# Kernel tuning notes

Hardware: AMD Instinct MI355X
Metric: run time of the kernel (lower is better)

Reference implementation:

```python
import jax, jax.numpy as jnp
import numpy as np

N_HEAD, D_K, D_V, D_MODEL = 8, 64, 64, 512
LN_EPS = 1e-5

def setup_inputs() -> dict:
    key = jax.random.key(0)
    k1, k2, k3 = jax.random.split(key, 3)
    B, C, H, W = 8, D_MODEL, 32, 32
    q = jax.random.normal(k1, (B, C, H, W), dtype=jnp.float32)
    w_qkvs = jax.random.normal(k2, (N_HEAD * D_K, D_MODEL), dtype=jnp.float32) * np.sqrt(2.0 / (D_MODEL + D_K))
    fc_w = jax.random.normal(k3, (D_MODEL, N_HEAD * D_V), dtype=jnp.float32) * np.sqrt(2.0 / (N_HEAD * D_V + D_MODEL))
    fc_b = jnp.zeros((D_MODEL,), dtype=jnp.float32)
    ln_gamma = jnp.ones((D_MODEL,), dtype=jnp.float32)
    ln_beta = jnp.zeros((D_MODEL,), dtype=jnp.float32)
    return {"q": q, "w_qkvs": w_qkvs, "fc_w": fc_w, "fc_b": fc_b,
            "ln_gamma": ln_gamma, "ln_beta": ln_beta}

def reference(q, w_qkvs, fc_w, fc_b, ln_gamma, ln_beta):
    B, C, H, W = q.shape
    L = H * W
    temp = np.sqrt(D_K).astype(np.float32)
    # [B, C, H, W] -> [B, L, C] tokens
    x = q.reshape(B, C, L).transpose(0, 2, 1)
    residual = x
    # shared QKV projection -> per-head [B, h, L, d]
    qh = (x @ w_qkvs.T).reshape(B, L, N_HEAD, D_K).transpose(0, 2, 1, 3)
    # self-attention: q = k = v = qh
    scores = jnp.einsum('bhqd,bhkd->bhqk', qh, qh) / temp
    attn = jax.nn.softmax(scores, axis=-1)  # dropout is identity in eval
    out = jnp.einsum('bhqk,bhkd->bhqd', attn, qh)  # [B, h, L, d_v]
    # merge heads: [B, L, h*d_v]
    out = out.transpose(0, 2, 1, 3).reshape(B, L, N_HEAD * D_V)
    out = out @ fc_w.T + fc_b
    y = out + residual
    mu = jnp.mean(y, axis=-1, keepdims=True)
    var = jnp.mean(jnp.square(y - mu), axis=-1, keepdims=True)
    y = (y - mu) / jnp.sqrt(var + LN_EPS) * ln_gamma + ln_beta
    # raw reshape, matching torch .view(B, -1, H, W)
    return y.reshape(B, -1, H, W)
```

## Files before the change

### kernel.cpp

```cpp
#include <hip/hip_runtime.h>
#include <stdint.h>

#define BATCH 8
#define LTOK 1024
#define DMODEL 512
#define NHEAD 8
#define DHEAD 64

typedef unsigned short u16;
typedef u16 u16x8 __attribute__((ext_vector_type(8)));
typedef short bf16x8 __attribute__((ext_vector_type(8)));
typedef float f32x4 __attribute__((ext_vector_type(4)));

#define MFMA16(a,b,c) __builtin_amdgcn_mfma_f32_16x16x32_bf16((a),(b),(c),0,0,0)

__device__ __forceinline__ float bf2f(u16 x){
  union{unsigned u; float f;} v; v.u = ((unsigned)x)<<16; return v.f;
}
__device__ __forceinline__ u16 f2bf(float f){
  union{float f; unsigned u;} v; v.f = f;
  unsigned r = v.u + 0x7fffu + ((v.u>>16)&1u);
  return (u16)(r>>16);
}

__device__ __forceinline__ void gload_lds16(const u16* g, u16* l){
  __builtin_amdgcn_global_load_lds(
      (const __attribute__((address_space(1))) void*)g,
      (__attribute__((address_space(3))) void*)l,
      16, 0, 0);
}

__global__ __launch_bounds__(256) void convert_k(const float* __restrict__ src,
                                                 u16* __restrict__ dst, int n){
  const int i = (blockIdx.x*256 + threadIdx.x)*8;
  if (i >= n) return;
  u16x8 v;
  #pragma unroll
  for (int j=0;j<8;j++) v[j] = f2bf(src[i+j]);
  *(u16x8*)(dst + i) = v;
}

__global__ __launch_bounds__(256) void transpose_f2b(const float* __restrict__ src,
                                                     u16* __restrict__ dst,
                                                     int R, int C){
  __shared__ __align__(16) u16 t[64][72];
  const int b  = blockIdx.z;
  const int r0 = blockIdx.x*64, c0 = blockIdx.y*64;
  const float* s = src + (size_t)b*R*C;
  u16* d         = dst + (size_t)b*R*C;
  const int tid = threadIdx.x;
  const int row = tid>>3, ch = (tid&7)*8;
  #pragma unroll
  for (int rr=0; rr<64; rr+=32){
    const float* p = s + (size_t)(r0+row+rr)*C + c0 + ch;
    u16x8 v;
    #pragma unroll
    for (int j=0;j<8;j++) v[j] = f2bf(p[j]);
    *(u16x8*)&t[row+rr][ch] = v;
  }
  __syncthreads();
  #pragma unroll
  for (int rr=0; rr<64; rr+=32){
    const int dr = row+rr;
    u16x8 v;
    #pragma unroll
    for (int j=0;j<8;j++) v[j] = t[ch+j][dr];
    *(u16x8*)(d + (size_t)(c0+dr)*R + r0 + ch) = v;
  }
}

__device__ __forceinline__ void stage_gemm(const u16* __restrict__ src,
                                           int row0, int k0, u16* lds, int tid){
  #pragma unroll
  for (int s2=0; s2<2; ++s2){
    const int slot = tid + s2*256;
    const int row = slot>>3, ch8 = slot&7;
    const int k = k0 + ((ch8 ^ (row&7))<<3);
    gload_lds16(src + (size_t)(row0+row)*DMODEL + k, lds + slot*8);
  }
}

__global__ __launch_bounds__(256) void qkv_gemm(const u16* __restrict__ A,
                                                const u16* __restrict__ W,
                                                u16* __restrict__ Kf,
                                                u16* __restrict__ Vf){
  __shared__ __align__(128) u16 sA[2][4096];
  __shared__ __align__(128) u16 sB[2][4096];
  const int m0 = blockIdx.x*64, n0 = blockIdx.y*64;
  const int tid = threadIdx.x, w = tid>>6, lane = tid&63;
  const int wr = w>>1, wc = w&1;
  const int lr = lane&15, lg = lane>>4;
  f32x4 acc[2][2] = {};
  stage_gemm(A, m0, 0, sA[0], tid);
  stage_gemm(W, n0, 0, sB[0], tid);
  int buf = 0;
  for (int kt=0; kt<8; ++kt){
    __syncthreads();
    if (kt < 7){
      stage_gemm(A, m0, (kt+1)*64, sA[buf^1], tid);
      stage_gemm(W, n0, (kt+1)*64, sB[buf^1], tid);
    }
    #pragma unroll
    for (int ks=0; ks<2; ++ks){
      bf16x8 af[2], bfr[2];
      #pragma unroll
      for (int mi=0; mi<2; ++mi){
        const int r = wr*32 + mi*16 + lr;
        af[mi] = *(const bf16x8*)(&sA[buf][(r*64 + ks*32 + lg*8) ^ ((r&7)<<3)]);
      }
      #pragma unroll
      for (int nj=0; nj<2; ++nj){
        const int r = wc*32 + nj*16 + lr;
        bfr[nj] = *(const bf16x8*)(&sB[buf][(r*64 + ks*32 + lg*8) ^ ((r&7)<<3)]);
      }
      #pragma unroll
      for (int mi=0; mi<2; ++mi)
        #pragma unroll
        for (int nj=0; nj<2; ++nj)
          acc[mi][nj] = MFMA16(af[mi], bfr[nj], acc[mi][nj]);
    }
    buf ^= 1;
  }
  #pragma unroll
  for (int mi=0; mi<2; ++mi)
    #pragma unroll
    for (int nj=0; nj<2; ++nj)
      #pragma unroll
      for (int r=0; r<4; ++r){
        const int m = m0 + wr*32 + mi*16 + lg*4 + r;
        const int n = n0 + wc*32 + nj*16 + lr;
        const int bb = m>>10, l = m&1023, hh = n>>6, d = n&63;
        const int bh = bb*NHEAD + hh;
        const int t = l>>6;
        const u16 val = f2bf(acc[mi][nj][r]);
        {
          const int rr = l&63;
          const int fnj = rr>>4, flr = rr&15;
          const int fks = d>>5, flg = (d>>3)&3, fj = d&7;
          Kf[(size_t)(bh*16 + t)*4096 + (fks*4+fnj)*512 + (flg*16+flr)*8 + fj] = val;
        }
        {
          const int ll = l&63;
          const int fks = ll>>5, flg = (ll>>3)&3, fj = ll&7;
          const int fdj = d>>4, flr = d&15;
          Vf[(size_t)(bh*16 + t)*4096 + (fks*4+fdj)*512 + (flg*16+flr)*8 + fj] = val;
        }
      }
}

__global__ __launch_bounds__(256,1) void attn_k(const u16* __restrict__ kf,
                                                const u16* __restrict__ vf,
                                                u16* __restrict__ ao){
  __shared__ __align__(128) u16 sP[16384];
  const int bid = blockIdx.x;
  const int qt = bid >> 6, bh = bid & 63;
  const int b = bh >> 3, h = bh & 7;
  const u16* Kf = kf + (size_t)bh*16*4096;
  const u16* Vf = vf + (size_t)bh*16*4096;
  const int tid = threadIdx.x, w = tid>>6, lane = tid&63;
  const int lr = lane&15, lg = lane>>4;
  const int qtw = qt*4 + w;

  bf16x8 aq[4][2];
  #pragma unroll
  for (int g=0; g<4; ++g)
    #pragma unroll
    for (int ks=0; ks<2; ++ks){
      u16x8 v = *(const u16x8*)(Kf + (size_t)qtw*4096 + (ks*4+g)*512 + lane*8);
      bf16x8 t;
      #pragma unroll
      for (int j=0;j<8;j++) t[j] = (short)f2bf(bf2f(v[j])*0.18033688f);
      aq[g][ks] = t;
    }

  f32x4 o[4][4] = {};
  float lsum[4][4] = {};

  for (int kt=0; kt<16; ++kt){
    const u16* Kt = Kf + (size_t)kt*4096;
    const u16* Vt = Vf + (size_t)kt*4096;
    bf16x8 bk[2][4];
    #pragma unroll
    for (int ks=0; ks<2; ++ks)
      #pragma unroll
      for (int nj=0; nj<4; ++nj)
        bk[ks][nj] = *(const bf16x8*)(Kt + (ks*4+nj)*512 + lane*8);
    #pragma unroll
    for (int g=0; g<4; ++g){
      f32x4 sc[4] = {};
      __builtin_amdgcn_s_setprio(1);
      #pragma unroll
      for (int ks=0; ks<2; ++ks)
        #pragma unroll
        for (int nj=0; nj<4; ++nj)
          sc[nj] = MFMA16(aq[g][ks], bk[ks][nj], sc[nj]);
      __builtin_amdgcn_s_setprio(0);
      const int wp = (w*4+g)*1024;
      #pragma unroll
      for (int nj=0; nj<4; ++nj){
        #pragma unroll
        for (int r=0; r<4; ++r){
          const float p = __builtin_amdgcn_exp2f(sc[nj][r]);
          const unsigned pu = __float_as_uint(p) & 0xFFFF0000u;
          lsum[g][r] += __uint_as_float(pu);
          const int prow = lg*4 + r;
          sP[wp + ((prow*64 + nj*16 + lr) ^ ((prow&7)<<3))] = (u16)(pu>>16);
        }
      }
    }
    asm volatile("s_waitcnt lgkmcnt(0)" ::: "memory");
    bf16x8 bv[2][4];
    #pragma unroll
    for (int ks=0; ks<2; ++ks)
      #pragma unroll
      for (int dj=0; dj<4; ++dj)
        bv[ks][dj] = *(const bf16x8*)(Vt + (ks*4+dj)*512 + lane*8);
    __builtin_amdgcn_s_setprio(1);
    #pragma unroll
    for (int g=0; g<4; ++g){
      const int wp = (w*4+g)*1024;
      #pragma unroll
      for (int ks=0; ks<2; ++ks){
        bf16x8 pa = *(const bf16x8*)(&sP[wp + ((lr*64 + ks*32 + lg*8) ^ ((lr&7)<<3))]);
        #pragma unroll
        for (int dj=0; dj<4; ++dj)
          o[g][dj] = MFMA16(pa, bv[ks][dj], o[g][dj]);
      }
    }
    __builtin_amdgcn_s_setprio(0);
  }

  #pragma unroll
  for (int g=0; g<4; ++g){
    float inv[4];
    #pragma unroll
    for (int r=0; r<4; ++r){
      float s = lsum[g][r];
      s += __shfl_xor(s,1); s += __shfl_xor(s,2);
      s += __shfl_xor(s,4); s += __shfl_xor(s,8);
      inv[r] = __builtin_amdgcn_rcpf(s);
    }
    const int i0 = qtw*64 + g*16;
    #pragma unroll
    for (int dj=0; dj<4; ++dj)
      #pragma unroll
      for (int r=0; r<4; ++r){
        const int l = i0 + lg*4 + r;
        const int d = dj*16 + lr;
        ao[((size_t)(b*LTOK + l))*DMODEL + h*DHEAD + d] = f2bf(o[g][dj][r]*inv[r]);
      }
  }
}

__global__ __launch_bounds__(256) void fc_gemm(const u16* __restrict__ A,
                                               const u16* __restrict__ W,
                                               const float* __restrict__ bias,
                                               const u16* __restrict__ resid,
                                               u16* __restrict__ Y){
  __shared__ __align__(128) u16 sA[2][4096];
  __shared__ __align__(128) u16 sB[2][4096];
  const int m0 = blockIdx.x*64, n0 = blockIdx.y*64;
  const int tid = threadIdx.x, w = tid>>6, lane = tid&63;
  const int wr = w>>1, wc = w&1;
  const int lr = lane&15, lg = lane>>4;
  f32x4 acc[2][2] = {};
  stage_gemm(A, m0, 0, sA[0], tid);
  stage_gemm(W, n0, 0, sB[0], tid);
  int buf = 0;
  for (int kt=0; kt<8; ++kt){
    __syncthreads();
    if (kt < 7){
      stage_gemm(A, m0, (kt+1)*64, sA[buf^1], tid);
      stage_gemm(W, n0, (kt+1)*64, sB[buf^1], tid);
    }
    #pragma unroll
    for (int ks=0; ks<2; ++ks){
      bf16x8 af[2], bfr[2];
      #pragma unroll
      for (int mi=0; mi<2; ++mi){
        const int r = wr*32 + mi*16 + lr;
        af[mi] = *(const bf16x8*)(&sA[buf][(r*64 + ks*32 + lg*8) ^ ((r&7)<<3)]);
      }
      #pragma unroll
      for (int nj=0; nj<2; ++nj){
        const int r = wc*32 + nj*16 + lr;
        bfr[nj] = *(const bf16x8*)(&sB[buf][(r*64 + ks*32 + lg*8) ^ ((r&7)<<3)]);
      }
      #pragma unroll
      for (int mi=0; mi<2; ++mi)
        #pragma unroll
        for (int nj=0; nj<2; ++nj)
          acc[mi][nj] = MFMA16(af[mi], bfr[nj], acc[mi][nj]);
    }
    buf ^= 1;
  }
  #pragma unroll
  for (int mi=0; mi<2; ++mi)
    #pragma unroll
    for (int nj=0; nj<2; ++nj)
      #pragma unroll
      for (int r=0; r<4; ++r){
        const int m = m0 + wr*32 + mi*16 + lg*4 + r;
        const int n = n0 + wc*32 + nj*16 + lr;
        const float val = acc[mi][nj][r] + bias[n] + bf2f(resid[(size_t)m*DMODEL+n]);
        Y[(size_t)m*DMODEL+n] = f2bf(val);
      }
}

__global__ __launch_bounds__(256) void ln_k(const u16* __restrict__ Y,
                                            const float* __restrict__ gamma,
                                            const float* __restrict__ beta,
                                            float* __restrict__ out){
  const int row = blockIdx.x*4 + (threadIdx.x>>6);
  const int lane = threadIdx.x&63;
  const u16* yr = Y + (size_t)row*DMODEL;
  u16x8 v = *(const u16x8*)(yr + lane*8);
  float x[8]; float s=0.f, sq=0.f;
  #pragma unroll
  for (int j=0;j<8;j++){ x[j]=bf2f(v[j]); s+=x[j]; sq+=x[j]*x[j]; }
  #pragma unroll
  for (int mk=1; mk<64; mk<<=1){ s += __shfl_xor(s,mk); sq += __shfl_xor(sq,mk); }
  const float mean = s*(1.f/DMODEL);
  float var = sq*(1.f/DMODEL) - mean*mean;
  const float rstd = rsqrtf(var + 1e-5f);
  float* po = out + (size_t)row*DMODEL + lane*8;
  #pragma unroll
  for (int j=0;j<8;j++){
    const int c = lane*8+j;
    po[j] = (x[j]-mean)*rstd*gamma[c] + beta[c];
  }
}

extern "C" void kernel_launch(void* const* d_in, const int* in_sizes, int n_in,
                              void* d_out, int out_size, void* d_ws, size_t ws_size,
                              hipStream_t stream){
  (void)in_sizes; (void)n_in; (void)out_size; (void)ws_size;
  const float* q      = (const float*)d_in[0];
  const float* w_qkvs = (const float*)d_in[1];
  const float* fc_w   = (const float*)d_in[2];
  const float* fc_b   = (const float*)d_in[3];
  const float* ln_g   = (const float*)d_in[4];
  const float* ln_b   = (const float*)d_in[5];
  float* out = (float*)d_out;
  char* ws = (char*)d_ws;
  u16* x_rm  = (u16*)(ws);
  u16* kfb   = (u16*)(ws + 8388608);
  u16* vfb   = (u16*)(ws + 16777216);
  u16* ao    = (u16*)(ws + 25165824);
  u16* wqkvb = (u16*)(ws + 33554432);
  u16* wfcb  = (u16*)(ws + 34078720);
  u16* y0    = kfb;

  convert_k<<<128,256,0,stream>>>(w_qkvs, wqkvb, DMODEL*DMODEL);
  convert_k<<<128,256,0,stream>>>(fc_w,   wfcb,  DMODEL*DMODEL);
  transpose_f2b<<<dim3(8,16,BATCH),256,0,stream>>>(q, x_rm, DMODEL, LTOK);
  qkv_gemm<<<dim3(128,8),256,0,stream>>>(x_rm, wqkvb, kfb, vfb);
  attn_k<<<256,256,0,stream>>>(kfb, vfb, ao);
  fc_gemm<<<dim3(128,8),256,0,stream>>>(ao, wfcb, fc_b, x_rm, y0);
  ln_k<<<2048,256,0,stream>>>(y0, ln_g, ln_b, out);
}
```

Baseline: 81.67 us.

## Share double-buffered K/V tiles in LDS and halve attention work per block

The attention kernel now gives each block 128 queries instead of 256, so each wave owns 32 query rows, and the grid doubles to 512 blocks with two blocks per CU allowed. Each K/V tile is loaded once per block into LDS with async global-to-LDS copies, double-buffered so the next tile is fetched while the current one is computed. Before, every wave read K/V fragments straight from global memory. The aim is more waves in flight and less redundant global/L2 traffic. The cost is a block-wide barrier every key tile, plus more total K/V tile loads across the larger grid.

```diff
diff --git a/kernel.cpp b/kernel.cpp
--- a/kernel.cpp
+++ b/kernel.cpp
@@ -148,61 +148,77 @@
       }
 }
 
-__global__ __launch_bounds__(256,1) void attn_k(const u16* __restrict__ kf,
+__global__ __launch_bounds__(256,2) void attn_k(const u16* __restrict__ kf,
                                                 const u16* __restrict__ vf,
                                                 u16* __restrict__ ao){
-  __shared__ __align__(128) u16 sP[16384];
+  __shared__ __align__(128) u16 sK[2][4096];
+  __shared__ __align__(128) u16 sV[2][4096];
+  __shared__ __align__(128) u16 sP[8192];
   const int bid = blockIdx.x;
-  const int qt = bid >> 6, bh = bid & 63;
+  const int qq = bid >> 6, bh = bid & 63;
   const int b = bh >> 3, h = bh & 7;
   const u16* Kf = kf + (size_t)bh*16*4096;
   const u16* Vf = vf + (size_t)bh*16*4096;
   const int tid = threadIdx.x, w = tid>>6, lane = tid&63;
   const int lr = lane&15, lg = lane>>4;
-  const int qtw = qt*4 + w;
-
-  bf16x8 aq[4][2];
-  #pragma unroll
-  for (int g=0; g<4; ++g)
+  const int qtile = qq*2 + (w>>1);
+  const int g0 = (w&1)*2;
+
+  bf16x8 aq[2][2];
+  #pragma unroll
+  for (int gg=0; gg<2; ++gg)
     #pragma unroll
     for (int ks=0; ks<2; ++ks){
-      u16x8 v = *(const u16x8*)(Kf + (size_t)qtw*4096 + (ks*4+g)*512 + lane*8);
+      u16x8 v = *(const u16x8*)(Kf + (size_t)qtile*4096 + (ks*4+g0+gg)*512 + lane*8);
       bf16x8 t;
       #pragma unroll
       for (int j=0;j<8;j++) t[j] = (short)f2bf(bf2f(v[j])*0.18033688f);
-      aq[g][ks] = t;
-    }
-
-  f32x4 o[4][4] = {};
-  float lsum[4][4] = {};
-
+      aq[gg][ks] = t;
+    }
+
+  f32x4 o[2][4] = {};
+  float lsum[2][4] = {};
+
+  gload_lds16(Kf + tid*8,        sK[0] + tid*8);
+  gload_lds16(Kf + 2048 + tid*8, sK[0] + 2048 + tid*8);
+  gload_lds16(Vf + tid*8,        sV[0] + tid*8);
+  gload_lds16(Vf + 2048 + tid*8, sV[0] + 2048 + tid*8);
+  __syncthreads();
+
+  int buf = 0;
   for (int kt=0; kt<16; ++kt){
-    const u16* Kt = Kf + (size_t)kt*4096;
-    const u16* Vt = Vf + (size_t)kt*4096;
+    if (kt+1 < 16){
+      const u16* Kn = Kf + (size_t)(kt+1)*4096;
+      const u16* Vn = Vf + (size_t)(kt+1)*4096;
+      gload_lds16(Kn + tid*8,        sK[buf^1] + tid*8);
+      gload_lds16(Kn + 2048 + tid*8, sK[buf^1] + 2048 + tid*8);
+      gload_lds16(Vn + tid*8,        sV[buf^1] + tid*8);
+      gload_lds16(Vn + 2048 + tid*8, sV[buf^1] + 2048 + tid*8);
+    }
     bf16x8 bk[2][4];
     #pragma unroll
     for (int ks=0; ks<2; ++ks)
       #pragma unroll
       for (int nj=0; nj<4; ++nj)
-        bk[ks][nj] = *(const bf16x8*)(Kt + (ks*4+nj)*512 + lane*8);
-    #pragma unroll
-    for (int g=0; g<4; ++g){
+        bk[ks][nj] = *(const bf16x8*)(&sK[buf][(ks*4+nj)*512 + lane*8]);
+    #pragma unroll
+    for (int gg=0; gg<2; ++gg){
       f32x4 sc[4] = {};
       __builtin_amdgcn_s_setprio(1);
       #pragma unroll
       for (int ks=0; ks<2; ++ks)
         #pragma unroll
         for (int nj=0; nj<4; ++nj)
-          sc[nj] = MFMA16(aq[g][ks], bk[ks][nj], sc[nj]);
+          sc[nj] = MFMA16(aq[gg][ks], bk[ks][nj], sc[nj]);
       __builtin_amdgcn_s_setprio(0);
-      const int wp = (w*4+g)*1024;
+      const int wp = (w*2+gg)*1024;
       #pragma unroll
       for (int nj=0; nj<4; ++nj){
         #pragma unroll
         for (int r=0; r<4; ++r){
           const float p = __builtin_amdgcn_exp2f(sc[nj][r]);
           const unsigned pu = __float_as_uint(p) & 0xFFFF0000u;
-          lsum[g][r] += __uint_as_float(pu);
+          lsum[gg][r] += __uint_as_float(pu);
           const int prow = lg*4 + r;
           sP[wp + ((prow*64 + nj*16 + lr) ^ ((prow&7)<<3))] = (u16)(pu>>16);
         }
@@ -214,40 +230,42 @@
     for (int ks=0; ks<2; ++ks)
       #pragma unroll
       for (int dj=0; dj<4; ++dj)
-        bv[ks][dj] = *(const bf16x8*)(Vt + (ks*4+dj)*512 + lane*8);
+        bv[ks][dj] = *(const bf16x8*)(&sV[buf][(ks*4+dj)*512 + lane*8]);
     __builtin_amdgcn_s_setprio(1);
     #pragma unroll
-    for (int g=0; g<4; ++g){
-      const int wp = (w*4+g)*1024;
+    for (int gg=0; gg<2; ++gg){
+      const int wp = (w*2+gg)*1024;
       #pragma unroll
       for (int ks=0; ks<2; ++ks){
         bf16x8 pa = *(const bf16x8*)(&sP[wp + ((lr*64 + ks*32 + lg*8) ^ ((lr&7)<<3))]);
         #pragma unroll
         for (int dj=0; dj<4; ++dj)
-          o[g][dj] = MFMA16(pa, bv[ks][dj], o[g][dj]);
+          o[gg][dj] = MFMA16(pa, bv[ks][dj], o[gg][dj]);
       }
     }
     __builtin_amdgcn_s_setprio(0);
-  }
-
-  #pragma unroll
-  for (int g=0; g<4; ++g){
+    __syncthreads();
+    buf ^= 1;
+  }
+
+  #pragma unroll
+  for (int gg=0; gg<2; ++gg){
     float inv[4];
     #pragma unroll
     for (int r=0; r<4; ++r){
-      float s = lsum[g][r];
+      float s = lsum[gg][r];
       s += __shfl_xor(s,1); s += __shfl_xor(s,2);
       s += __shfl_xor(s,4); s += __shfl_xor(s,8);
       inv[r] = __builtin_amdgcn_rcpf(s);
     }
-    const int i0 = qtw*64 + g*16;
+    const int i0 = qtile*64 + (g0+gg)*16;
     #pragma unroll
     for (int dj=0; dj<4; ++dj)
       #pragma unroll
       for (int r=0; r<4; ++r){
         const int l = i0 + lg*4 + r;
         const int d = dj*16 + lr;
-        ao[((size_t)(b*LTOK + l))*DMODEL + h*DHEAD + d] = f2bf(o[g][dj][r]*inv[r]);
+        ao[((size_t)(b*LTOK + l))*DMODEL + h*DHEAD + d] = f2bf(o[gg][dj][r]*inv[r]);
       }
   }
 }
@@ -355,7 +373,7 @@
   convert_k<<<128,256,0,stream>>>(fc_w,   wfcb,  DMODEL*DMODEL);
   transpose_f2b<<<dim3(8,16,BATCH),256,0,stream>>>(q, x_rm, DMODEL, LTOK);
   qkv_gemm<<<dim3(128,8),256,0,stream>>>(x_rm, wqkvb, kfb, vfb);
-  attn_k<<<256,256,0,stream>>>(kfb, vfb, ao);
+  attn_k<<<512,256,0,stream>>>(kfb, vfb, ao);
   fc_gemm<<<dim3(128,8),256,0,stream>>>(ao, wfcb, fc_b, x_rm, y0);
   ln_k<<<2048,256,0,stream>>>(y0, ln_g, ln_b, out);
 }
```

Measured after the change: 77.48 us. -5.1%, faster.

## Split attention KV loop across waves and merge partial outputs in LDS

Applied to the files above, without the earlier changes.

Each attention block now owns a single 64-row query tile, and its four waves each process a quarter of the key/value tiles rather than each wave covering all 16 tiles for its own query tile. The grid grows from 256 to 1024 blocks and launch bounds allow 4 blocks per CU, so each CU runs more waves to hide memory and MFMA latency. Because the softmax uses no running max, the partial outputs and row sums can simply be added, which is done through a two-step LDS tree reduction before wave 0 normalises and writes. This adds barriers, extra LDS traffic and redundant Q loading per block.

```diff
diff --git a/kernel.cpp b/kernel.cpp
--- a/kernel.cpp
+++ b/kernel.cpp
@@ -148,10 +148,10 @@
       }
 }
 
-__global__ __launch_bounds__(256,1) void attn_k(const u16* __restrict__ kf,
+__global__ __launch_bounds__(256,4) void attn_k(const u16* __restrict__ kf,
                                                 const u16* __restrict__ vf,
                                                 u16* __restrict__ ao){
-  __shared__ __align__(128) u16 sP[16384];
+  __shared__ __align__(16) u16 sPm[16640];
   const int bid = blockIdx.x;
   const int qt = bid >> 6, bh = bid & 63;
   const int b = bh >> 3, h = bh & 7;
@@ -159,14 +159,13 @@
   const u16* Vf = vf + (size_t)bh*16*4096;
   const int tid = threadIdx.x, w = tid>>6, lane = tid&63;
   const int lr = lane&15, lg = lane>>4;
-  const int qtw = qt*4 + w;
 
   bf16x8 aq[4][2];
   #pragma unroll
   for (int g=0; g<4; ++g)
     #pragma unroll
     for (int ks=0; ks<2; ++ks){
-      u16x8 v = *(const u16x8*)(Kf + (size_t)qtw*4096 + (ks*4+g)*512 + lane*8);
+      u16x8 v = *(const u16x8*)(Kf + (size_t)qt*4096 + (ks*4+g)*512 + lane*8);
       bf16x8 t;
       #pragma unroll
       for (int j=0;j<8;j++) t[j] = (short)f2bf(bf2f(v[j])*0.18033688f);
@@ -176,7 +175,8 @@
   f32x4 o[4][4] = {};
   float lsum[4][4] = {};
 
-  for (int kt=0; kt<16; ++kt){
+  for (int t=0; t<4; ++t){
+    const int kt = w + t*4;
     const u16* Kt = Kf + (size_t)kt*4096;
     const u16* Vt = Vf + (size_t)kt*4096;
     bf16x8 bk[2][4];
@@ -204,7 +204,7 @@
           const unsigned pu = __float_as_uint(p) & 0xFFFF0000u;
           lsum[g][r] += __uint_as_float(pu);
           const int prow = lg*4 + r;
-          sP[wp + ((prow*64 + nj*16 + lr) ^ ((prow&7)<<3))] = (u16)(pu>>16);
+          sPm[wp + ((prow*64 + nj*16 + lr) ^ ((prow&7)<<3))] = (u16)(pu>>16);
         }
       }
     }
@@ -221,7 +221,7 @@
       const int wp = (w*4+g)*1024;
       #pragma unroll
       for (int ks=0; ks<2; ++ks){
-        bf16x8 pa = *(const bf16x8*)(&sP[wp + ((lr*64 + ks*32 + lg*8) ^ ((lr&7)<<3))]);
+        bf16x8 pa = *(const bf16x8*)(&sPm[wp + ((lr*64 + ks*32 + lg*8) ^ ((lr&7)<<3))]);
         #pragma unroll
         for (int dj=0; dj<4; ++dj)
           o[g][dj] = MFMA16(pa, bv[ks][dj], o[g][dj]);
@@ -231,24 +231,79 @@
   }
 
   #pragma unroll
-  for (int g=0; g<4; ++g){
-    float inv[4];
+  for (int g=0; g<4; ++g)
     #pragma unroll
     for (int r=0; r<4; ++r){
       float s = lsum[g][r];
       s += __shfl_xor(s,1); s += __shfl_xor(s,2);
       s += __shfl_xor(s,4); s += __shfl_xor(s,8);
-      inv[r] = __builtin_amdgcn_rcpf(s);
-    }
-    const int i0 = qtw*64 + g*16;
-    #pragma unroll
-    for (int dj=0; dj<4; ++dj)
-      #pragma unroll
-      for (int r=0; r<4; ++r){
-        const int l = i0 + lg*4 + r;
-        const int d = dj*16 + lr;
-        ao[((size_t)(b*LTOK + l))*DMODEL + h*DHEAD + d] = f2bf(o[g][dj][r]*inv[r]);
-      }
+      lsum[g][r] = s;
+    }
+
+  __syncthreads();
+  float* mrg = (float*)sPm;
+  if (w & 1){
+    float* R = mrg + (w>>1)*4160;
+    #pragma unroll
+    for (int g=0; g<4; ++g){
+      #pragma unroll
+      for (int dj=0; dj<4; ++dj)
+        *(f32x4*)&R[(g*4+dj)*256 + lane*4] = o[g][dj];
+      if (lr == 0)
+        #pragma unroll
+        for (int r=0; r<4; ++r) R[4096 + g*16 + lg*4 + r] = lsum[g][r];
+    }
+  }
+  __syncthreads();
+  if (!(w & 1)){
+    float* R = mrg + (w>>1)*4160;
+    #pragma unroll
+    for (int g=0; g<4; ++g){
+      #pragma unroll
+      for (int dj=0; dj<4; ++dj)
+        o[g][dj] += *(const f32x4*)&R[(g*4+dj)*256 + lane*4];
+      #pragma unroll
+      for (int r=0; r<4; ++r) lsum[g][r] += R[4096 + g*16 + lg*4 + r];
+    }
+  }
+  if (w == 2){
+    float* R = mrg + 4160;
+    #pragma unroll
+    for (int g=0; g<4; ++g){
+      #pragma unroll
+      for (int dj=0; dj<4; ++dj)
+        *(f32x4*)&R[(g*4+dj)*256 + lane*4] = o[g][dj];
+      if (lr == 0)
+        #pragma unroll
+        for (int r=0; r<4; ++r) R[4096 + g*16 + lg*4 + r] = lsum[g][r];
+    }
+  }
+  __syncthreads();
+  if (w == 0){
+    float* R = mrg + 4160;
+    #pragma unroll
+    for (int g=0; g<4; ++g){
+      #pragma unroll
+      for (int dj=0; dj<4; ++dj)
+        o[g][dj] += *(const f32x4*)&R[(g*4+dj)*256 + lane*4];
+      #pragma unroll
+      for (int r=0; r<4; ++r) lsum[g][r] += R[4096 + g*16 + lg*4 + r];
+    }
+    #pragma unroll
+    for (int g=0; g<4; ++g){
+      float inv[4];
+      #pragma unroll
+      for (int r=0; r<4; ++r) inv[r] = __builtin_amdgcn_rcpf(lsum[g][r]);
+      const int i0 = qt*64 + g*16;
+      #pragma unroll
+      for (int dj=0; dj<4; ++dj)
+        #pragma unroll
+        for (int r=0; r<4; ++r){
+          const int l = i0 + lg*4 + r;
+          const int d = dj*16 + lr;
+          ao[((size_t)(b*LTOK + l))*DMODEL + h*DHEAD + d] = f2bf(o[g][dj][r]*inv[r]);
+        }
+    }
   }
 }
 
@@ -355,7 +410,7 @@
   convert_k<<<128,256,0,stream>>>(fc_w,   wfcb,  DMODEL*DMODEL);
   transpose_f2b<<<dim3(8,16,BATCH),256,0,stream>>>(q, x_rm, DMODEL, LTOK);
   qkv_gemm<<<dim3(128,8),256,0,stream>>>(x_rm, wqkvb, kfb, vfb);
-  attn_k<<<256,256,0,stream>>>(kfb, vfb, ao);
+  attn_k<<<1024,256,0,stream>>>(kfb, vfb, ao);
   fc_gemm<<<dim3(128,8),256,0,stream>>>(ao, wfcb, fc_b, x_rm, y0);
   ln_k<<<2048,256,0,stream>>>(y0, ln_g, ln_b, out);
 }
```

Result: slower. 145.4 us (+78.0%).
